# Kernel tuning notes

Measured on AMD Instinct MI355X. Metric: run time of the kernel, lower is better.

## Reference

```python
import jax, jax.numpy as jnp
import numpy as np

# ----- constants derived from SNNNetwork.__init__ kwargs -----
T, B = 500, 32                     # steps = sim_time/dt = 25/0.05
ARCH = [512, 1024, 512]
DT = 0.05
R = 1.0 / 9.43
I0 = 700.0
K_M = 1.0 / (R * I0 * DT)          # as in __init__: k_m = 1/(R*I0*dt)
THRESH = 10.0                      # fixed plausible threshold (torch code derives it from `target`, but is non-runnable)
SPIKE_R = 20.0
SIGMA_V = 10.0
V_RESET = 0.0
ASC_AMP = np.array([-9.18, -198.94], np.float32)
ASC_R = np.array([1.0, 1.0], np.float32)
ASC_K = np.array([0.003, 0.1], np.float32)


def setup_inputs() -> dict:
    key = jax.random.key(0)
    k1, k2, k3 = jax.random.split(key, 3)
    inputs = jax.random.normal(k1, (T, B, ARCH[0]), dtype=jnp.float32)
    # nn.init.uniform_(linear.weight, wt-1, wt+1); use small symmetric range
    W1 = jax.random.uniform(k2, (ARCH[1], ARCH[0]), jnp.float32, -0.05, 0.05)
    W2 = jax.random.uniform(k3, (ARCH[2], ARCH[1]), jnp.float32, -0.05, 0.05)
    return {"inputs": inputs, "W1": W1, "W2": W2}


def _neuron_step(state, x):
    """One GLIFR (rate-based GLIF with after-spike currents) update.
    state = (v [B,N], asc [2,B,N]); x is synaptic drive [B,N].
    Returns (new_state, spikes [B,N]).
    """
    v, asc = state
    amp = jnp.asarray(ASC_AMP)[:, None, None]
    rmul = jnp.asarray(ASC_R)[:, None, None]
    kasc = jnp.asarray(ASC_K)[:, None, None]
    syn = I0 * x                                          # k_syn = 1
    i_total = syn + asc.sum(0)
    s = SPIKE_R * jax.nn.sigmoid((v - THRESH) / SIGMA_V)  # smooth spike rate
    s_dt = s * DT
    asc_new = asc * (1.0 - DT * kasc) + s_dt * (rmul * asc + amp)
    v_new = v + DT * K_M * (R * i_total - (v - V_RESET)) + s_dt * (V_RESET - v)
    return (v_new, asc_new), s


def reference(inputs, W1, W2):
    Bc = inputs.shape[1]

    def zstate(n):
        return (jnp.zeros((Bc, n), inputs.dtype), jnp.zeros((2, Bc, n), inputs.dtype))

    init = (zstate(ARCH[0]), jnp.zeros((Bc, ARCH[0]), inputs.dtype),
            zstate(ARCH[1]), jnp.zeros((Bc, ARCH[1]), inputs.dtype),
            zstate(ARCH[2]))

    def step(carry, x):
        st0, buf0, st1, buf1, st2 = carry
        # layer 0: no linear, raw input drives the neuron
        st0, s0 = _neuron_step(st0, x)
        # layer 1: delayed (delay=1) spikes of layer 0 through Linear
        st1, s1 = _neuron_step(st1, buf0 @ W1.T)
        # layer 2: delayed spikes of layer 1 through Linear
        st2, s2 = _neuron_step(st2, buf1 @ W2.T)
        return (st0, s0, st1, s1, st2), s2

    _, spikes_all = jax.lax.scan(step, init, inputs)
    return spikes_all  # [T, B, ARCH[-1]] == layers[-1].spikes_all
```

## Files before the change

### kernel.cpp

```cpp
#include <hip/hip_runtime.h>
#include <hip/hip_bf16.h>
#include <stdint.h>

#define TSTEPS 500
#define BB 32
#define N0 512
#define N1 1024
#define N2 512

typedef unsigned short ushort_t;
typedef __attribute__((ext_vector_type(8))) short short8;
typedef __attribute__((ext_vector_type(4))) float f32x4;

__device__ __forceinline__ ushort_t f2b(float x) {
    union { float f; uint32_t u; } c; c.f = x;
    uint32_t r = (c.u + 0x7fffu + ((c.u >> 16) & 1u)) >> 16;
    return (ushort_t)r;
}
__device__ __forceinline__ float b2f(ushort_t u) {
    union { uint32_t u; float f; } c; c.u = ((uint32_t)u) << 16;
    return c.f;
}

__device__ __forceinline__ float glifr_step(float& v, float& a0, float& a1,
                                            float x) {
    const float INV_I0 = 1.0f / 700.0f;
    const float C2 = 9.43f / 700.0f;
    const float CE = 0.14426950408889634f;
    const float CE10 = 1.4426950408889634f;
    const float C0 = 1.0f - 0.05f * 0.003f;
    const float C1 = 1.0f - 0.05f * 0.1f;
    const float AMP0 = -9.18f, AMP1 = -198.94f;

    float asum = a0 + a1;
    float drv = fmaf(asum, INV_I0, x);
    float e = exp2f(fmaf(v, -CE, CE10));
    float sig = __builtin_amdgcn_rcpf(1.0f + e);
    float na0 = fmaf(sig, a0 + AMP0, a0 * C0);
    float na1 = fmaf(sig, a1 + AMP1, a1 * C1);
    float nv = fmaf(-sig, v, fmaf(-C2, v, v + drv));
    a0 = na0; a1 = na1; v = nv;
    return sig;
}

#define PD 20
template <int NW, int MODE>
__device__ __forceinline__ void scan_body(const float* __restrict__ drive,
                                          uint32_t* __restrict__ pout,
                                          float* __restrict__ fout, int idx) {
    const int S = BB * NW;

    auto LD = [&](int t) -> float {
        if (MODE == 0) return drive[(size_t)t * S + idx];
        return (t == 0) ? 0.0f : drive[(size_t)(t - 1) * S + idx];
    };

    float v = 0.f, a0 = 0.f, a1 = 0.f;

    auto STEP = [&](int t, float x) {
        float sig = glifr_step(v, a0, a1, x);
        size_t o = (size_t)t * S + idx;
        if (MODE == 2) {
            fout[o] = 20.0f * sig;
        } else {
            ushort_t hi = f2b(sig);
            float lo = sig - b2f(hi);
            pout[o] = (uint32_t)hi | ((uint32_t)f2b(lo) << 16);
        }
    };

    float p[PD];
#pragma unroll
    for (int i = 0; i < PD; ++i) p[i] = LD(i);

    for (int t = 0; t < TSTEPS - PD; t += PD) {
        float q[PD];
#pragma unroll
        for (int i = 0; i < PD; ++i) q[i] = LD(t + PD + i);
#pragma unroll
        for (int i = 0; i < PD; ++i) STEP(t + i, p[i]);
#pragma unroll
        for (int i = 0; i < PD; ++i) p[i] = q[i];
    }
#pragma unroll
    for (int i = 0; i < PD; ++i) STEP(TSTEPS - PD + i, p[i]);
}

__global__ void scan0_wsplit(const float* __restrict__ inputs,
                             uint32_t* __restrict__ s0,
                             const float* __restrict__ W1,
                             const float* __restrict__ W2,
                             ushort_t* __restrict__ w1h, ushort_t* __restrict__ w1l,
                             ushort_t* __restrict__ w2h, ushort_t* __restrict__ w2l) {
    const int bid = blockIdx.x;
    if (bid < (BB * N0) / 64) {
        scan_body<N0, 0>(inputs, s0, nullptr, bid * 64 + threadIdx.x);
    } else {
        int i = (bid - (BB * N0) / 64) * 64 + threadIdx.x;
        float a = 20.0f * W1[i];
        ushort_t h = f2b(a);
        w1h[i] = h; w1l[i] = f2b(a - b2f(h));
        float b = 20.0f * W2[i];
        h = f2b(b);
        w2h[i] = h; w2l[i] = f2b(b - b2f(h));
    }
}

template <int NW>
__global__ void scan_mid(const float* __restrict__ drive,
                         uint32_t* __restrict__ sout) {
    scan_body<NW, 1>(drive, sout, nullptr,
                     blockIdx.x * blockDim.x + threadIdx.x);
}

__global__ void scan_last(const float* __restrict__ drive,
                          float* __restrict__ out) {
    scan_body<N2, 2>(drive, nullptr, out,
                     blockIdx.x * blockDim.x + threadIdx.x);
}

template <int NBY>
__global__ __launch_bounds__(256, 2) void gemm_x3(
    const uint32_t* __restrict__ Apk,
    const ushort_t* __restrict__ Bh, const ushort_t* __restrict__ Bl,
    float* __restrict__ C, int Ncols, int K) {
    __shared__ char lds[65536];
    const int tid = threadIdx.x;
    const int lane = tid & 63, wave = tid >> 6;

    const int id = blockIdx.x, nwg = gridDim.x;
    const int qq = nwg >> 3, rr = nwg & 7;
    const int xcd = id & 7, jj = id >> 3;
    const int wg = (xcd < rr ? xcd * (qq + 1) : rr * (qq + 1) + (xcd - rr) * qq) + jj;
    const int m0 = (wg / NBY) * 128;
    const int n0 = (wg % NBY) * 128;

    const ushort_t* gB = (wave == 2) ? Bh : Bl;
    const int chunk_sw = (lane & 3) ^ ((lane >> 3) & 3);
    const size_t rowbB = (size_t)K * 2;
    const char* gsrcB = (const char*)gB +
                        (size_t)(n0 + (lane >> 2)) * rowbB + (size_t)chunk_sw * 16;

    const int r0 = tid >> 3, c4 = tid & 7;
    const int ch = (c4 >> 1) ^ ((r0 >> 1) & 3);
    const int aoff = r0 * 64 + ch * 16 + (c4 & 1) * 8;
    const uint32_t* aSrc = Apk + (size_t)(m0 + r0) * K + c4 * 4;

    const int KSTEPS = K / 32;

    f32x4 acc[4][4];
#pragma unroll
    for (int i = 0; i < 4; ++i)
#pragma unroll
        for (int j = 0; j < 4; ++j) acc[i][j] = (f32x4){0.f, 0.f, 0.f, 0.f};

    const int wm = wave >> 1, wn = wave & 1;
    const int r4 = lane & 15, kg = lane >> 4;
    const int slot = kg ^ ((r4 >> 1) & 3);
    const int fA = (wm * 64 + r4) * 64 + slot * 16;
    const int fB = (wn * 64 + r4) * 64 + slot * 16;

    auto issueB = [&](int ks, int base) {
#pragma unroll
        for (int i = 0; i < 8; ++i) {
            __builtin_amdgcn_global_load_lds(
                (const __attribute__((address_space(1))) uint32_t*)(
                    gsrcB + (size_t)i * 16 * rowbB + (size_t)ks * 64),
                (__attribute__((address_space(3))) uint32_t*)(
                    lds + base + 16384 + (wave - 2) * 8192 + i * 1024),
                16, 0, 0);
        }
    };
    auto loadA = [&](int ks, uint4* pk) {
#pragma unroll
        for (int i = 0; i < 4; ++i)
            pk[i] = *reinterpret_cast<const uint4*>(
                aSrc + (size_t)i * 32 * K + (size_t)ks * 32);
    };
    auto writeA = [&](const uint4* pk, int base) {
#pragma unroll
        for (int i = 0; i < 4; ++i) {
            uint32_t hi01 = __builtin_amdgcn_perm(pk[i].y, pk[i].x, 0x05040100u);
            uint32_t lo01 = __builtin_amdgcn_perm(pk[i].y, pk[i].x, 0x07060302u);
            uint32_t hi23 = __builtin_amdgcn_perm(pk[i].w, pk[i].z, 0x05040100u);
            uint32_t lo23 = __builtin_amdgcn_perm(pk[i].w, pk[i].z, 0x07060302u);
            *reinterpret_cast<uint2*>(lds + base + aoff + i * 2048) =
                make_uint2(hi01, hi23);
            *reinterpret_cast<uint2*>(lds + base + 8192 + aoff + i * 2048) =
                make_uint2(lo01, lo23);
        }
    };
    auto compute = [&](int base) {
        short8 ah[4], al[4], bh[4], bl[4];
#pragma unroll
        for (int i = 0; i < 4; ++i) {
            ah[i] = *(const short8*)(lds + base + 0     + fA + i * 1024);
            al[i] = *(const short8*)(lds + base + 8192  + fA + i * 1024);
            bh[i] = *(const short8*)(lds + base + 16384 + fB + i * 1024);
            bl[i] = *(const short8*)(lds + base + 24576 + fB + i * 1024);
        }
#pragma unroll
        for (int i = 0; i < 4; ++i)
#pragma unroll
            for (int j = 0; j < 4; ++j) {
                acc[i][j] = __builtin_amdgcn_mfma_f32_16x16x32_bf16(
                    ah[i], bh[j], acc[i][j], 0, 0, 0);
                acc[i][j] = __builtin_amdgcn_mfma_f32_16x16x32_bf16(
                    ah[i], bl[j], acc[i][j], 0, 0, 0);
                acc[i][j] = __builtin_amdgcn_mfma_f32_16x16x32_bf16(
                    al[i], bh[j], acc[i][j], 0, 0, 0);
            }
    };

    {
        if (wave >= 2) issueB(0, 0);
        uint4 pk[4];
        loadA(0, pk);
        writeA(pk, 0);
        __syncthreads();
    }

    for (int ks = 0; ks < KSTEPS; ks += 2) {
        {
            if (wave >= 2) issueB(ks + 1, 32768);
            uint4 pk[4];
            loadA(ks + 1, pk);
            compute(0);
            writeA(pk, 32768);
            __syncthreads();
        }
        {
            const bool more = (ks + 2 < KSTEPS);
            uint4 pk[4];
            if (wave >= 2 && more) issueB(ks + 2, 0);
            if (more) loadA(ks + 2, pk);
            compute(32768);
            if (more) writeA(pk, 0);
            __syncthreads();
        }
    }

#pragma unroll
    for (int i = 0; i < 4; ++i)
#pragma unroll
        for (int j = 0; j < 4; ++j)
#pragma unroll
            for (int r = 0; r < 4; ++r) {
                int row = m0 + wm * 64 + i * 16 + kg * 4 + r;
                int col = n0 + wn * 64 + j * 16 + r4;
                C[(size_t)row * Ncols + col] = acc[i][j][r];
            }
}

extern "C" void kernel_launch(void* const* d_in, const int* in_sizes, int n_in,
                              void* d_out, int out_size, void* d_ws,
                              size_t ws_size, hipStream_t stream) {
    const float* inputs = (const float*)d_in[0];
    const float* W1 = (const float*)d_in[1];
    const float* W2 = (const float*)d_in[2];
    float* out = (float*)d_out;
    char* ws = (char*)d_ws;

    uint32_t* s0 = (uint32_t*)ws;
    uint32_t* s1 = (uint32_t*)ws;
    float*    x1 = (float*)(ws + 65536000);
    float*    x2 = (float*)(ws + 65536000);
    ushort_t* w1h = (ushort_t*)(ws + 131072000);
    ushort_t* w1l = (ushort_t*)(ws + 132120576);
    ushort_t* w2h = (ushort_t*)(ws + 133169152);
    ushort_t* w2l = (ushort_t*)(ws + 134217728);

    scan0_wsplit<<<256 + 8192, 64, 0, stream>>>(inputs, s0, W1, W2,
                                                w1h, w1l, w2h, w2l);
    gemm_x3<8><<<1000, 256, 0, stream>>>(s0, w1h, w1l, x1, N1, N0);
    scan_mid<N1><<<512, 64, 0, stream>>>(x1, s1);
    gemm_x3<4><<<500, 256, 0, stream>>>(s1, w2h, w2l, x2, N2, N1);
    scan_last<<<256, 64, 0, stream>>>(x2, out);
}
```

Baseline: 211.7 us.

## Load A fragments directly into registers, bypassing LDS in split-bf16 GEMM

After: 274.6 us. 29.7% more time.

```diff
diff --git a/kernel.cpp b/kernel.cpp
--- a/kernel.cpp
+++ b/kernel.cpp
@@ -43,7 +43,7 @@
     return sig;
 }
 
-#define PD 20
+#define PD 25
 template <int NW, int MODE>
 __device__ __forceinline__ void scan_body(const float* __restrict__ drive,
                                           uint32_t* __restrict__ pout,
@@ -119,12 +119,13 @@
                      blockIdx.x * blockDim.x + threadIdx.x);
 }
 
-template <int NBY>
+template <int NBY, int KC>
 __global__ __launch_bounds__(256, 2) void gemm_x3(
     const uint32_t* __restrict__ Apk,
     const ushort_t* __restrict__ Bh, const ushort_t* __restrict__ Bl,
-    float* __restrict__ C, int Ncols, int K) {
-    __shared__ char lds[65536];
+    float* __restrict__ C) {
+    constexpr int NC = NBY * 128;
+    __shared__ char lds[32768];
     const int tid = threadIdx.x;
     const int lane = tid & 63, wave = tid >> 6;
 
@@ -137,28 +138,24 @@
 
     const ushort_t* gB = (wave == 2) ? Bh : Bl;
     const int chunk_sw = (lane & 3) ^ ((lane >> 3) & 3);
-    const size_t rowbB = (size_t)K * 2;
+    const size_t rowbB = (size_t)KC * 2;
     const char* gsrcB = (const char*)gB +
                         (size_t)(n0 + (lane >> 2)) * rowbB + (size_t)chunk_sw * 16;
-
-    const int r0 = tid >> 3, c4 = tid & 7;
-    const int ch = (c4 >> 1) ^ ((r0 >> 1) & 3);
-    const int aoff = r0 * 64 + ch * 16 + (c4 & 1) * 8;
-    const uint32_t* aSrc = Apk + (size_t)(m0 + r0) * K + c4 * 4;
-
-    const int KSTEPS = K / 32;
-
-    f32x4 acc[4][4];
-#pragma unroll
-    for (int i = 0; i < 4; ++i)
-#pragma unroll
-        for (int j = 0; j < 4; ++j) acc[i][j] = (f32x4){0.f, 0.f, 0.f, 0.f};
 
     const int wm = wave >> 1, wn = wave & 1;
     const int r4 = lane & 15, kg = lane >> 4;
     const int slot = kg ^ ((r4 >> 1) & 3);
-    const int fA = (wm * 64 + r4) * 64 + slot * 16;
     const int fB = (wn * 64 + r4) * 64 + slot * 16;
+
+    const uint32_t* aFrag = Apk + (size_t)(m0 + wm * 64 + r4) * KC + kg * 8;
+
+    const int KSTEPS = KC / 32;
+
+    f32x4 acc[4][4];
+#pragma unroll
+    for (int i = 0; i < 4; ++i)
+#pragma unroll
+        for (int j = 0; j < 4; ++j) acc[i][j] = (f32x4){0.f, 0.f, 0.f, 0.f};
 
     auto issueB = [&](int ks, int base) {
 #pragma unroll
@@ -167,77 +164,72 @@
                 (const __attribute__((address_space(1))) uint32_t*)(
                     gsrcB + (size_t)i * 16 * rowbB + (size_t)ks * 64),
                 (__attribute__((address_space(3))) uint32_t*)(
-                    lds + base + 16384 + (wave - 2) * 8192 + i * 1024),
+                    lds + base + (wave - 2) * 8192 + i * 1024),
                 16, 0, 0);
         }
     };
     auto loadA = [&](int ks, uint4* pk) {
 #pragma unroll
-        for (int i = 0; i < 4; ++i)
-            pk[i] = *reinterpret_cast<const uint4*>(
-                aSrc + (size_t)i * 32 * K + (size_t)ks * 32);
-    };
-    auto writeA = [&](const uint4* pk, int base) {
-#pragma unroll
         for (int i = 0; i < 4; ++i) {
-            uint32_t hi01 = __builtin_amdgcn_perm(pk[i].y, pk[i].x, 0x05040100u);
-            uint32_t lo01 = __builtin_amdgcn_perm(pk[i].y, pk[i].x, 0x07060302u);
-            uint32_t hi23 = __builtin_amdgcn_perm(pk[i].w, pk[i].z, 0x05040100u);
-            uint32_t lo23 = __builtin_amdgcn_perm(pk[i].w, pk[i].z, 0x07060302u);
-            *reinterpret_cast<uint2*>(lds + base + aoff + i * 2048) =
-                make_uint2(hi01, hi23);
-            *reinterpret_cast<uint2*>(lds + base + 8192 + aoff + i * 2048) =
-                make_uint2(lo01, lo23);
-        }
-    };
-    auto compute = [&](int base) {
-        short8 ah[4], al[4], bh[4], bl[4];
+            pk[2 * i] = *reinterpret_cast<const uint4*>(
+                aFrag + (size_t)i * 16 * KC + ks * 32);
+            pk[2 * i + 1] = *reinterpret_cast<const uint4*>(
+                aFrag + (size_t)i * 16 * KC + ks * 32 + 4);
+        }
+    };
+    auto compute = [&](const uint4* pk, int base) {
+        short8 bh[4], bl[4];
+#pragma unroll
+        for (int j = 0; j < 4; ++j) {
+            bh[j] = *(const short8*)(lds + base + fB + j * 1024);
+            bl[j] = *(const short8*)(lds + base + 8192 + fB + j * 1024);
+        }
 #pragma unroll
         for (int i = 0; i < 4; ++i) {
-            ah[i] = *(const short8*)(lds + base + 0     + fA + i * 1024);
-            al[i] = *(const short8*)(lds + base + 8192  + fA + i * 1024);
-            bh[i] = *(const short8*)(lds + base + 16384 + fB + i * 1024);
-            bl[i] = *(const short8*)(lds + base + 24576 + fB + i * 1024);
-        }
-#pragma unroll
-        for (int i = 0; i < 4; ++i)
+            const uint4 p0 = pk[2 * i], p1 = pk[2 * i + 1];
+            uint32_t h[4], l[4];
+            h[0] = __builtin_amdgcn_perm(p0.y, p0.x, 0x05040100u);
+            h[1] = __builtin_amdgcn_perm(p0.w, p0.z, 0x05040100u);
+            h[2] = __builtin_amdgcn_perm(p1.y, p1.x, 0x05040100u);
+            h[3] = __builtin_amdgcn_perm(p1.w, p1.z, 0x05040100u);
+            l[0] = __builtin_amdgcn_perm(p0.y, p0.x, 0x07060302u);
+            l[1] = __builtin_amdgcn_perm(p0.w, p0.z, 0x07060302u);
+            l[2] = __builtin_amdgcn_perm(p1.y, p1.x, 0x07060302u);
+            l[3] = __builtin_amdgcn_perm(p1.w, p1.z, 0x07060302u);
+            short8 ah, al;
+            uint32_t* ahp = reinterpret_cast<uint32_t*>(&ah);
+            uint32_t* alp = reinterpret_cast<uint32_t*>(&al);
+            ahp[0] = h[0]; ahp[1] = h[1]; ahp[2] = h[2]; ahp[3] = h[3];
+            alp[0] = l[0]; alp[1] = l[1]; alp[2] = l[2]; alp[3] = l[3];
 #pragma unroll
             for (int j = 0; j < 4; ++j) {
                 acc[i][j] = __builtin_amdgcn_mfma_f32_16x16x32_bf16(
-                    ah[i], bh[j], acc[i][j], 0, 0, 0);
+                    ah, bh[j], acc[i][j], 0, 0, 0);
                 acc[i][j] = __builtin_amdgcn_mfma_f32_16x16x32_bf16(
-                    ah[i], bl[j], acc[i][j], 0, 0, 0);
+                    ah, bl[j], acc[i][j], 0, 0, 0);
                 acc[i][j] = __builtin_amdgcn_mfma_f32_16x16x32_bf16(
-                    al[i], bh[j], acc[i][j], 0, 0, 0);
+                    al, bh[j], acc[i][j], 0, 0, 0);
             }
-    };
-
-    {
-        if (wave >= 2) issueB(0, 0);
-        uint4 pk[4];
-        loadA(0, pk);
-        writeA(pk, 0);
+        }
+    };
+
+    uint4 pk[8], pkN[8];
+    if (wave >= 2) issueB(0, 0);
+    loadA(0, pk);
+    __syncthreads();
+
+    for (int ks = 0; ks < KSTEPS; ks += 2) {
+        if (wave >= 2) issueB(ks + 1, 16384);
+        loadA(ks + 1, pkN);
+        compute(pk, 0);
         __syncthreads();
-    }
-
-    for (int ks = 0; ks < KSTEPS; ks += 2) {
-        {
-            if (wave >= 2) issueB(ks + 1, 32768);
-            uint4 pk[4];
-            loadA(ks + 1, pk);
-            compute(0);
-            writeA(pk, 32768);
-            __syncthreads();
-        }
-        {
-            const bool more = (ks + 2 < KSTEPS);
-            uint4 pk[4];
-            if (wave >= 2 && more) issueB(ks + 2, 0);
-            if (more) loadA(ks + 2, pk);
-            compute(32768);
-            if (more) writeA(pk, 0);
-            __syncthreads();
-        }
+        const bool more = (ks + 2 < KSTEPS);
+        if (more) {
+            if (wave >= 2) issueB(ks + 2, 0);
+            loadA(ks + 2, pk);
+        }
+        compute(pkN, 16384);
+        __syncthreads();
     }
 
 #pragma unroll
@@ -248,7 +240,7 @@
             for (int r = 0; r < 4; ++r) {
                 int row = m0 + wm * 64 + i * 16 + kg * 4 + r;
                 int col = n0 + wn * 64 + j * 16 + r4;
-                C[(size_t)row * Ncols + col] = acc[i][j][r];
+                C[(size_t)row * NC + col] = acc[i][j][r];
             }
 }
 
@@ -272,8 +264,8 @@
 
     scan0_wsplit<<<256 + 8192, 64, 0, stream>>>(inputs, s0, W1, W2,
                                                 w1h, w1l, w2h, w2l);
-    gemm_x3<8><<<1000, 256, 0, stream>>>(s0, w1h, w1l, x1, N1, N0);
+    gemm_x3<8, N0><<<1000, 256, 0, stream>>>(s0, w1h, w1l, x1);
     scan_mid<N1><<<512, 64, 0, stream>>>(x1, s1);
-    gemm_x3<4><<<500, 256, 0, stream>>>(s1, w2h, w2l, x2, N2, N1);
+    gemm_x3<4, N1><<<500, 256, 0, stream>>>(s1, w2h, w2l, x2);
     scan_last<<<256, 64, 0, stream>>>(x2, out);
 }
```

## Triple-buffer B tiles in split-bf16 GEMM and specialize K at compile time

Applied to the files above, without the earlier changes.

Result: faster. 202.1 us (-4.6%).

```diff
diff --git a/kernel.cpp b/kernel.cpp
--- a/kernel.cpp
+++ b/kernel.cpp
@@ -43,7 +43,7 @@
     return sig;
 }
 
-#define PD 20
+#define PD 25
 template <int NW, int MODE>
 __device__ __forceinline__ void scan_body(const float* __restrict__ drive,
                                           uint32_t* __restrict__ pout,
@@ -63,9 +63,9 @@
         if (MODE == 2) {
             fout[o] = 20.0f * sig;
         } else {
-            ushort_t hi = f2b(sig);
-            float lo = sig - b2f(hi);
-            pout[o] = (uint32_t)hi | ((uint32_t)f2b(lo) << 16);
+            uint32_t su = __float_as_uint(sig);
+            float lo = sig - __uint_as_float(su & 0xffff0000u);
+            pout[o] = (su >> 16) | (__float_as_uint(lo) & 0xffff0000u);
         }
     };
 
@@ -119,12 +119,14 @@
                      blockIdx.x * blockDim.x + threadIdx.x);
 }
 
-template <int NBY>
+template <int NBY, int KC>
 __global__ __launch_bounds__(256, 2) void gemm_x3(
     const uint32_t* __restrict__ Apk,
     const ushort_t* __restrict__ Bh, const ushort_t* __restrict__ Bl,
-    float* __restrict__ C, int Ncols, int K) {
-    __shared__ char lds[65536];
+    float* __restrict__ C) {
+    constexpr int NC = NBY * 128;
+    constexpr int KSTEPS = KC / 32;
+    __shared__ char lds[81920];
     const int tid = threadIdx.x;
     const int lane = tid & 63, wave = tid >> 6;
 
@@ -137,22 +139,14 @@
 
     const ushort_t* gB = (wave == 2) ? Bh : Bl;
     const int chunk_sw = (lane & 3) ^ ((lane >> 3) & 3);
-    const size_t rowbB = (size_t)K * 2;
+    const size_t rowbB = (size_t)KC * 2;
     const char* gsrcB = (const char*)gB +
                         (size_t)(n0 + (lane >> 2)) * rowbB + (size_t)chunk_sw * 16;
 
     const int r0 = tid >> 3, c4 = tid & 7;
     const int ch = (c4 >> 1) ^ ((r0 >> 1) & 3);
     const int aoff = r0 * 64 + ch * 16 + (c4 & 1) * 8;
-    const uint32_t* aSrc = Apk + (size_t)(m0 + r0) * K + c4 * 4;
-
-    const int KSTEPS = K / 32;
-
-    f32x4 acc[4][4];
-#pragma unroll
-    for (int i = 0; i < 4; ++i)
-#pragma unroll
-        for (int j = 0; j < 4; ++j) acc[i][j] = (f32x4){0.f, 0.f, 0.f, 0.f};
+    const uint32_t* aSrc = Apk + (size_t)(m0 + r0) * KC + c4 * 4;
 
     const int wm = wave >> 1, wn = wave & 1;
     const int r4 = lane & 15, kg = lane >> 4;
@@ -160,44 +154,52 @@
     const int fA = (wm * 64 + r4) * 64 + slot * 16;
     const int fB = (wn * 64 + r4) * 64 + slot * 16;
 
-    auto issueB = [&](int ks, int base) {
-#pragma unroll
-        for (int i = 0; i < 8; ++i) {
-            __builtin_amdgcn_global_load_lds(
-                (const __attribute__((address_space(1))) uint32_t*)(
-                    gsrcB + (size_t)i * 16 * rowbB + (size_t)ks * 64),
-                (__attribute__((address_space(3))) uint32_t*)(
-                    lds + base + 16384 + (wave - 2) * 8192 + i * 1024),
-                16, 0, 0);
-        }
-    };
-    auto loadA = [&](int ks, uint4* pk) {
+    f32x4 acc[4][4];
+#pragma unroll
+    for (int i = 0; i < 4; ++i)
+#pragma unroll
+        for (int j = 0; j < 4; ++j) acc[i][j] = (f32x4){0.f, 0.f, 0.f, 0.f};
+
+    auto issueB = [&](int ks, int bbuf) {
+        if (wave >= 2) {
+#pragma unroll
+            for (int i = 0; i < 8; ++i) {
+                __builtin_amdgcn_global_load_lds(
+                    (const __attribute__((address_space(1))) uint32_t*)(
+                        gsrcB + (size_t)i * 16 * rowbB + (size_t)ks * 64),
+                    (__attribute__((address_space(3))) uint32_t*)(
+                        lds + 32768 + bbuf * 16384 + (wave - 2) * 8192 + i * 1024),
+                    16, 0, 0);
+            }
+        }
+    };
+    auto loadA = [&](int ks, uint4* R) {
 #pragma unroll
         for (int i = 0; i < 4; ++i)
-            pk[i] = *reinterpret_cast<const uint4*>(
-                aSrc + (size_t)i * 32 * K + (size_t)ks * 32);
-    };
-    auto writeA = [&](const uint4* pk, int base) {
+            R[i] = *reinterpret_cast<const uint4*>(
+                aSrc + (size_t)i * 32 * KC + (size_t)ks * 32);
+    };
+    auto writeA = [&](const uint4* R, int abuf) {
 #pragma unroll
         for (int i = 0; i < 4; ++i) {
-            uint32_t hi01 = __builtin_amdgcn_perm(pk[i].y, pk[i].x, 0x05040100u);
-            uint32_t lo01 = __builtin_amdgcn_perm(pk[i].y, pk[i].x, 0x07060302u);
-            uint32_t hi23 = __builtin_amdgcn_perm(pk[i].w, pk[i].z, 0x05040100u);
-            uint32_t lo23 = __builtin_amdgcn_perm(pk[i].w, pk[i].z, 0x07060302u);
-            *reinterpret_cast<uint2*>(lds + base + aoff + i * 2048) =
+            uint32_t hi01 = __builtin_amdgcn_perm(R[i].y, R[i].x, 0x05040100u);
+            uint32_t lo01 = __builtin_amdgcn_perm(R[i].y, R[i].x, 0x07060302u);
+            uint32_t hi23 = __builtin_amdgcn_perm(R[i].w, R[i].z, 0x05040100u);
+            uint32_t lo23 = __builtin_amdgcn_perm(R[i].w, R[i].z, 0x07060302u);
+            *reinterpret_cast<uint2*>(lds + abuf * 16384 + aoff + i * 2048) =
                 make_uint2(hi01, hi23);
-            *reinterpret_cast<uint2*>(lds + base + 8192 + aoff + i * 2048) =
+            *reinterpret_cast<uint2*>(lds + abuf * 16384 + 8192 + aoff + i * 2048) =
                 make_uint2(lo01, lo23);
         }
     };
-    auto compute = [&](int base) {
+    auto compute = [&](int abuf, int bbuf) {
         short8 ah[4], al[4], bh[4], bl[4];
 #pragma unroll
         for (int i = 0; i < 4; ++i) {
-            ah[i] = *(const short8*)(lds + base + 0     + fA + i * 1024);
-            al[i] = *(const short8*)(lds + base + 8192  + fA + i * 1024);
-            bh[i] = *(const short8*)(lds + base + 16384 + fB + i * 1024);
-            bl[i] = *(const short8*)(lds + base + 24576 + fB + i * 1024);
+            ah[i] = *(const short8*)(lds + abuf * 16384 + fA + i * 1024);
+            al[i] = *(const short8*)(lds + abuf * 16384 + 8192 + fA + i * 1024);
+            bh[i] = *(const short8*)(lds + 32768 + bbuf * 16384 + fB + i * 1024);
+            bl[i] = *(const short8*)(lds + 32768 + bbuf * 16384 + 8192 + fB + i * 1024);
         }
 #pragma unroll
         for (int i = 0; i < 4; ++i)
@@ -211,34 +213,41 @@
                     al[i], bh[j], acc[i][j], 0, 0, 0);
             }
     };
-
-    {
-        if (wave >= 2) issueB(0, 0);
-        uint4 pk[4];
-        loadA(0, pk);
-        writeA(pk, 0);
-        __syncthreads();
+    auto bar = [&]() {
+        asm volatile("s_waitcnt lgkmcnt(0)" ::: "memory");
+        __builtin_amdgcn_s_barrier();
+        __builtin_amdgcn_sched_barrier(0);
+    };
+
+    uint4 R0[4], R1[4];
+    issueB(0, 0);
+    issueB(1, 1);
+    loadA(0, R0);
+    loadA(1, R1);
+    writeA(R0, 0);
+    bar();
+
+    int cB = 0;
+    for (int s = 0; s + 3 < KSTEPS; s += 2) {
+        int cB1 = cB + 1; if (cB1 == 3) cB1 = 0;
+        int cB2 = cB1 + 1; if (cB2 == 3) cB2 = 0;
+        issueB(s + 2, cB2);
+        loadA(s + 2, R0);
+        compute(0, cB);
+        writeA(R1, 1);
+        bar();
+        issueB(s + 3, cB);
+        loadA(s + 3, R1);
+        compute(1, cB1);
+        writeA(R0, 0);
+        bar();
+        cB = cB2;
     }
-
-    for (int ks = 0; ks < KSTEPS; ks += 2) {
-        {
-            if (wave >= 2) issueB(ks + 1, 32768);
-            uint4 pk[4];
-            loadA(ks + 1, pk);
-            compute(0);
-            writeA(pk, 32768);
-            __syncthreads();
-        }
-        {
-            const bool more = (ks + 2 < KSTEPS);
-            uint4 pk[4];
-            if (wave >= 2 && more) issueB(ks + 2, 0);
-            if (more) loadA(ks + 2, pk);
-            compute(32768);
-            if (more) writeA(pk, 0);
-            __syncthreads();
-        }
-    }
+    int cB1 = cB + 1; if (cB1 == 3) cB1 = 0;
+    compute(0, cB);
+    writeA(R1, 1);
+    bar();
+    compute(1, cB1);
 
 #pragma unroll
     for (int i = 0; i < 4; ++i)
@@ -248,7 +257,7 @@
             for (int r = 0; r < 4; ++r) {
                 int row = m0 + wm * 64 + i * 16 + kg * 4 + r;
                 int col = n0 + wn * 64 + j * 16 + r4;
-                C[(size_t)row * Ncols + col] = acc[i][j][r];
+                C[(size_t)row * NC + col] = acc[i][j][r];
             }
 }
 
@@ -272,8 +281,8 @@
 
     scan0_wsplit<<<256 + 8192, 64, 0, stream>>>(inputs, s0, W1, W2,
                                                 w1h, w1l, w2h, w2l);
-    gemm_x3<8><<<1000, 256, 0, stream>>>(s0, w1h, w1l, x1, N1, N0);
+    gemm_x3<8, N0><<<1000, 256, 0, stream>>>(s0, w1h, w1l, x1);
     scan_mid<N1><<<512, 64, 0, stream>>>(x1, s1);
-    gemm_x3<4><<<500, 256, 0, stream>>>(s1, w2h, w2l, x2, N2, N1);
+    gemm_x3<4, N1><<<500, 256, 0, stream>>>(s1, w2h, w2l, x2);
     scan_last<<<256, 64, 0, stream>>>(x2, out);
 }
```
